# Kernel optimization log

Measured on AMD Instinct MI355X. Metric: run time of the kernel, lower is better.

## Reference

```python
import jax, jax.numpy as jnp
import numpy as np

N_NODES = 100000
N_EDGES = 3200000
N_GRAPHS = 256
NFEAT = 256
NHID = 256
NCLASS = 16


def setup_inputs() -> dict:
    key = jax.random.key(0)
    ks = jax.random.split(key, 8)
    feats = jax.random.normal(ks[0], (N_NODES, NFEAT), dtype=jnp.float32)
    edge_src = jax.random.randint(ks[1], (N_EDGES,), 0, N_NODES, dtype=jnp.int32)
    edge_dst = jax.random.randint(ks[2], (N_EDGES,), 0, N_NODES, dtype=jnp.int32)
    graph_ids = jnp.sort(jax.random.randint(ks[3], (N_NODES,), 0, N_GRAPHS, dtype=jnp.int32))
    def glorot(k, shape):
        lim = float(np.sqrt(6.0 / (shape[0] + shape[1])))
        return jax.random.uniform(k, shape, dtype=jnp.float32, minval=-lim, maxval=lim)
    return {
        "features": feats,
        "edge_src": edge_src,
        "edge_dst": edge_dst,
        "graph_ids": graph_ids,
        "W1": glorot(ks[4], (NFEAT, NHID)), "b1": jnp.zeros((NHID,), jnp.float32),
        "W2": glorot(ks[5], (NHID, NHID)), "b2": jnp.zeros((NHID,), jnp.float32),
        "W3": glorot(ks[6], (NHID, NHID)), "b3": jnp.zeros((NHID,), jnp.float32),
        "Wlin": glorot(ks[7], (NHID, NCLASS)), "blin": jnp.zeros((NCLASS,), jnp.float32),
    }


def _degree_norms(edge_src, edge_dst):
    ones = jnp.ones((N_EDGES,), jnp.float32)
    out_deg = jax.ops.segment_sum(ones, edge_src, num_segments=N_NODES)
    in_deg = jax.ops.segment_sum(ones, edge_dst, num_segments=N_NODES)
    # DGL norm='both': D_out^{-1/2} on source side, D_in^{-1/2} on dest side
    norm_src = jnp.where(out_deg > 0, jax.lax.rsqrt(jnp.maximum(out_deg, 1.0)), 0.0)
    norm_dst = jnp.where(in_deg > 0, jax.lax.rsqrt(jnp.maximum(in_deg, 1.0)), 0.0)
    return norm_src, norm_dst


def _graph_conv(x, W, b, edge_src, edge_dst, norm_src, norm_dst):
    h = x @ W                                  # [N, out]
    msg = (h * norm_src[:, None])[edge_src]    # [E, out] gather
    agg = jax.ops.segment_sum(msg, edge_dst, num_segments=N_NODES)  # scatter-add
    return jax.nn.relu(agg * norm_dst[:, None] + b)


def reference(features, edge_src, edge_dst, graph_ids, W1, b1, W2, b2, W3, b3, Wlin, blin):
    norm_src, norm_dst = _degree_norms(edge_src, edge_dst)
    h = _graph_conv(features, W1, b1, edge_src, edge_dst, norm_src, norm_dst)
    # dropout is identity in eval mode
    h = _graph_conv(h, W2, b2, edge_src, edge_dst, norm_src, norm_dst)
    h = _graph_conv(h, W3, b3, edge_src, edge_dst, norm_src, norm_dst)
    # AvgPooling: mean of node features per graph
    sums = jax.ops.segment_sum(h, graph_ids, num_segments=N_GRAPHS)
    counts = jax.ops.segment_sum(jnp.ones((N_NODES,), jnp.float32), graph_ids, num_segments=N_GRAPHS)
    hg = sums / jnp.maximum(counts, 1.0)[:, None]   # [G, nhid]
    logits = hg @ Wlin + blin                        # [G, nclass]
    return jax.nn.log_softmax(logits, axis=1)
```

## Files before the change

kernel.cpp:

```cpp
#include <hip/hip_runtime.h>
#include <math.h>


#define HID 256

static __device__ __forceinline__ unsigned short f2bf(float f) {
    unsigned int u = __float_as_uint(f);
    unsigned int r = (u + 0x7fff + ((u >> 16) & 1)) >> 16;
    return (unsigned short)r;
}
static __device__ __forceinline__ float bf2f(unsigned short v) {
    return __uint_as_float(((unsigned int)v) << 16);
}

__global__ void k_degree_rank(const int* __restrict__ src, const int* __restrict__ dst,
                              int* __restrict__ outd, int* __restrict__ ind,
                              int* __restrict__ rank, int E) {
    int tid = blockIdx.x * blockDim.x + threadIdx.x;
    int stride = gridDim.x * blockDim.x;
    int E4 = E >> 2;
    const int4* src4 = (const int4*)src;
    const int4* dst4 = (const int4*)dst;
    int4* rank4 = (int4*)rank;
    for (int i = tid; i < E4; i += stride) {
        int4 s = src4[i], d = dst4[i];
        atomicAdd(&outd[s.x], 1); atomicAdd(&outd[s.y], 1);
        atomicAdd(&outd[s.z], 1); atomicAdd(&outd[s.w], 1);
        int4 r;
        r.x = atomicAdd(&ind[d.x], 1);
        r.y = atomicAdd(&ind[d.y], 1);
        r.z = atomicAdd(&ind[d.z], 1);
        r.w = atomicAdd(&ind[d.w], 1);
        rank4[i] = r;
    }
    for (int i = E4 * 4 + tid; i < E; i += stride) {
        atomicAdd(&outd[src[i]], 1);
        rank[i] = atomicAdd(&ind[dst[i]], 1);
    }
}

__global__ __launch_bounds__(256) void k_scan_part(const int* __restrict__ ind,
                                                   int* __restrict__ part, int N) {
    int b = blockIdx.x, t = threadIdx.x;
    int CH = (N + 255) / 256;
    int lo = b * CH, hi = min(N, lo + CH);
    int s = 0;
    for (int i = lo + t; i < hi; i += 256) s += ind[i];
    __shared__ int sm[256];
    sm[t] = s; __syncthreads();
    for (int o = 128; o; o >>= 1) { if (t < o) sm[t] += sm[t + o]; __syncthreads(); }
    if (!t) part[b] = sm[0];
}

__global__ __launch_bounds__(256) void k_scan_top(int* __restrict__ part) {
    int t = threadIdx.x;
    __shared__ int sm[256];
    int v = part[t];
    sm[t] = v; __syncthreads();
    for (int o = 1; o < 256; o <<= 1) {
        int u = (t >= o) ? sm[t - o] : 0;
        __syncthreads();
        sm[t] += u;
        __syncthreads();
    }
    part[t] = sm[t] - v;
}

__global__ __launch_bounds__(256) void k_scan_fill(const int* __restrict__ ind,
                                                   const int* __restrict__ outd,
                                                   const int* __restrict__ part,
                                                   int* __restrict__ offs,
                                                   float* __restrict__ ns,
                                                   float* __restrict__ nd, int N) {
    int b = blockIdx.x, t = threadIdx.x;
    int CH = (N + 255) / 256;
    int lo = b * CH, hi = min(N, lo + CH);
    __shared__ int sm[256];
    int base = part[b];
    for (int s0 = lo; s0 < hi; s0 += 256) {
        int i = s0 + t;
        int v = (i < hi) ? ind[i] : 0;
        sm[t] = v; __syncthreads();
        for (int o = 1; o < 256; o <<= 1) {
            int u = (t >= o) ? sm[t - o] : 0;
            __syncthreads();
            sm[t] += u;
            __syncthreads();
        }
        if (i < hi) {
            offs[i] = base + sm[t] - v;
            int od = outd[i];
            ns[i] = od > 0 ? rsqrtf((float)od) : 0.f;
            nd[i] = v > 0 ? rsqrtf((float)v) : 0.f;
        }
        base += sm[255];
        __syncthreads();
    }
    if (b == 255 && t == 0) offs[N] = base;
}

__global__ void k_fill(const int* __restrict__ src, const int* __restrict__ dst,
                       const int* __restrict__ rank, const int* __restrict__ offs,
                       int* __restrict__ csr, int E) {
    int tid = blockIdx.x * blockDim.x + threadIdx.x;
    int stride = gridDim.x * blockDim.x;
    int E4 = E >> 2;
    const int4* src4 = (const int4*)src;
    const int4* dst4 = (const int4*)dst;
    const int4* rank4 = (const int4*)rank;
    for (int i = tid; i < E4; i += stride) {
        int4 s = src4[i], d = dst4[i], r = rank4[i];
        csr[offs[d.x] + r.x] = s.x;
        csr[offs[d.y] + r.y] = s.y;
        csr[offs[d.z] + r.z] = s.z;
        csr[offs[d.w] + r.w] = s.w;
    }
    for (int i = E4 * 4 + tid; i < E; i += stride)
        csr[offs[dst[i]] + rank[i]] = src[i];
}

__global__ __launch_bounds__(256) void k_gemm(const float* __restrict__ A,
                                              const float* __restrict__ B,
                                              const float* __restrict__ ns,
                                              unsigned short* __restrict__ C, int M) {
    __shared__ float As[16][132];
    __shared__ float Bs[16][132];
    int t = threadIdx.x;
    int tx = t & 15, ty = t >> 4;
    int row0 = blockIdx.x * 128;
    int col0 = blockIdx.y * 128;
    float c[8][8] = {};
    for (int k0 = 0; k0 < 256; k0 += 16) {
        {
            int ar = t >> 1;
            int ak = (t & 1) * 8;
            int grow = row0 + ar;
            float4 a0 = make_float4(0.f, 0.f, 0.f, 0.f), a1 = a0;
            if (grow < M) {
                a0 = *(const float4*)&A[(size_t)grow * 256 + k0 + ak];
                a1 = *(const float4*)&A[(size_t)grow * 256 + k0 + ak + 4];
            }
            As[ak + 0][ar] = a0.x; As[ak + 1][ar] = a0.y;
            As[ak + 2][ar] = a0.z; As[ak + 3][ar] = a0.w;
            As[ak + 4][ar] = a1.x; As[ak + 5][ar] = a1.y;
            As[ak + 6][ar] = a1.z; As[ak + 7][ar] = a1.w;
        }
        {
            int br = t >> 4;
            int bc = (t & 15) * 8;
            float4 b0 = *(const float4*)&B[(size_t)(k0 + br) * 256 + col0 + bc];
            float4 b1 = *(const float4*)&B[(size_t)(k0 + br) * 256 + col0 + bc + 4];
            *(float4*)&Bs[br][bc] = b0;
            *(float4*)&Bs[br][bc + 4] = b1;
        }
        __syncthreads();
#pragma unroll
        for (int k = 0; k < 16; ++k) {
            float a[8], b[8];
            *(float4*)&a[0] = *(float4*)&As[k][ty * 4];
            *(float4*)&a[4] = *(float4*)&As[k][64 + ty * 4];
            *(float4*)&b[0] = *(float4*)&Bs[k][tx * 4];
            *(float4*)&b[4] = *(float4*)&Bs[k][64 + tx * 4];
#pragma unroll
            for (int i = 0; i < 8; ++i)
#pragma unroll
                for (int j = 0; j < 8; ++j)
                    c[i][j] = fmaf(a[i], b[j], c[i][j]);
        }
        __syncthreads();
    }
#pragma unroll
    for (int i = 0; i < 8; ++i) {
        int grow = row0 + ((i < 4) ? (ty * 4 + i) : (64 + ty * 4 + i - 4));
        if (grow < M) {
            float s = ns[grow];
            ushort4 v0, v1;
            v0.x = f2bf(c[i][0] * s); v0.y = f2bf(c[i][1] * s);
            v0.z = f2bf(c[i][2] * s); v0.w = f2bf(c[i][3] * s);
            v1.x = f2bf(c[i][4] * s); v1.y = f2bf(c[i][5] * s);
            v1.z = f2bf(c[i][6] * s); v1.w = f2bf(c[i][7] * s);
            *(ushort4*)&C[(size_t)grow * 256 + col0 + tx * 4] = v0;
            *(ushort4*)&C[(size_t)grow * 256 + col0 + 64 + tx * 4] = v1;
        }
    }
}

__global__ __launch_bounds__(256) void k_agg(const unsigned short* __restrict__ h,
                                             const int* __restrict__ csr,
                                             const int* __restrict__ offs,
                                             const float* __restrict__ nd,
                                             const float* __restrict__ bias,
                                             float* __restrict__ out, int N) {
    int wave = threadIdx.x >> 6;
    int lane = threadIdx.x & 63;
    int node = blockIdx.x * 4 + wave;
    if (node >= N) return;
    int e0 = offs[node], e1 = offs[node + 1];
    float acc0 = 0.f, acc1 = 0.f, acc2 = 0.f, acc3 = 0.f;
    int e = e0;
    for (; e + 1 < e1; e += 2) {
        int s0 = csr[e], s1 = csr[e + 1];
        ushort4 a = *(const ushort4*)&h[(size_t)s0 * 256 + lane * 4];
        ushort4 b = *(const ushort4*)&h[(size_t)s1 * 256 + lane * 4];
        acc0 += bf2f(a.x); acc1 += bf2f(a.y); acc2 += bf2f(a.z); acc3 += bf2f(a.w);
        acc0 += bf2f(b.x); acc1 += bf2f(b.y); acc2 += bf2f(b.z); acc3 += bf2f(b.w);
    }
    if (e < e1) {
        int s0 = csr[e];
        ushort4 a = *(const ushort4*)&h[(size_t)s0 * 256 + lane * 4];
        acc0 += bf2f(a.x); acc1 += bf2f(a.y); acc2 += bf2f(a.z); acc3 += bf2f(a.w);
    }
    float sc = nd[node];
    float4 b4 = *(const float4*)&bias[lane * 4];
    float4 r;
    r.x = fmaxf(fmaf(acc0, sc, b4.x), 0.f);
    r.y = fmaxf(fmaf(acc1, sc, b4.y), 0.f);
    r.z = fmaxf(fmaf(acc2, sc, b4.z), 0.f);
    r.w = fmaxf(fmaf(acc3, sc, b4.w), 0.f);
    *(float4*)&out[(size_t)node * 256 + lane * 4] = r;
}

__global__ __launch_bounds__(256) void k_pool(const float* __restrict__ h,
                                              const int* __restrict__ gid,
                                              const float* __restrict__ Wlin,
                                              const float* __restrict__ blin,
                                              float* __restrict__ out, int N) {
    int g = blockIdx.x;
    int t = threadIdx.x;
    int s, e;
    {
        int lo = 0, hi = N;
        while (lo < hi) { int m = (lo + hi) >> 1; if (gid[m] < g) lo = m + 1; else hi = m; }
        s = lo;
        lo = s; hi = N;
        while (lo < hi) { int m = (lo + hi) >> 1; if (gid[m] < g + 1) lo = m + 1; else hi = m; }
        e = lo;
    }
    float acc = 0.f;
    for (int i = s; i < e; ++i) acc += h[(size_t)i * 256 + t];
    float cntf = (float)((e - s) > 0 ? (e - s) : 1);
    __shared__ float hg[256];
    hg[t] = acc / cntf;
    __syncthreads();
    if (t < 16) {
        float v = blin[t];
        for (int k = 0; k < 256; ++k) v = fmaf(hg[k], Wlin[k * 16 + t], v);
        float m = v;
#pragma unroll
        for (int off = 8; off; off >>= 1) m = fmaxf(m, __shfl_xor(m, off, 16));
        float ex = expf(v - m);
        float ssum = ex;
#pragma unroll
        for (int off = 8; off; off >>= 1) ssum += __shfl_xor(ssum, off, 16);
        out[g * 16 + t] = v - m - logf(ssum);
    }
}

extern "C" void kernel_launch(void* const* d_in, const int* in_sizes, int n_in,
                              void* d_out, int out_size, void* d_ws, size_t ws_size,
                              hipStream_t stream) {
    const float* feats   = (const float*)d_in[0];
    const int*   edge_src= (const int*)d_in[1];
    const int*   edge_dst= (const int*)d_in[2];
    const int*   gid     = (const int*)d_in[3];
    const float* W1 = (const float*)d_in[4];  const float* b1 = (const float*)d_in[5];
    const float* W2 = (const float*)d_in[6];  const float* b2 = (const float*)d_in[7];
    const float* W3 = (const float*)d_in[8];  const float* b3 = (const float*)d_in[9];
    const float* Wlin = (const float*)d_in[10]; const float* blin = (const float*)d_in[11];
    float* out = (float*)d_out;

    const int E = in_sizes[1];
    const int N = in_sizes[3];
    const int G = 256;

    size_t off = 0;
    auto alloc = [&](size_t bytes) -> void* {
        void* p = (char*)d_ws + off;
        off += (bytes + 255) & ~(size_t)255;
        return p;
    };
    int*   outd = (int*)alloc((size_t)N * 4);
    int*   ind  = (int*)alloc((size_t)N * 4);
    size_t zero_bytes = off;
    int*   part = (int*)alloc(256 * 4);
    int*   offs = (int*)alloc(((size_t)N + 1) * 4);
    float* ns   = (float*)alloc((size_t)N * 4);
    float* nd   = (float*)alloc((size_t)N * 4);
    int*   csr  = (int*)alloc((size_t)E * 4);
    unsigned short* htmp = (unsigned short*)alloc((size_t)N * HID * 2);
    float* buf  = (float*)alloc((size_t)N * HID * 4);
    int*   rank = (int*)buf;
    (void)ws_size;

    hipMemsetAsync(d_ws, 0, zero_bytes, stream);

    k_degree_rank<<<2048, 256, 0, stream>>>(edge_src, edge_dst, outd, ind, rank, E);
    k_scan_part<<<256, 256, 0, stream>>>(ind, part, N);
    k_scan_top<<<1, 256, 0, stream>>>(part);
    k_scan_fill<<<256, 256, 0, stream>>>(ind, outd, part, offs, ns, nd, N);
    k_fill<<<2048, 256, 0, stream>>>(edge_src, edge_dst, rank, offs, csr, E);

    dim3 ggrid((N + 127) / 128, 2);
    int agg_blocks = (N + 3) / 4;

    k_gemm<<<ggrid, 256, 0, stream>>>(feats, W1, ns, htmp, N);
    k_agg<<<agg_blocks, 256, 0, stream>>>(htmp, csr, offs, nd, b1, buf, N);
    k_gemm<<<ggrid, 256, 0, stream>>>(buf, W2, ns, htmp, N);
    k_agg<<<agg_blocks, 256, 0, stream>>>(htmp, csr, offs, nd, b2, buf, N);
    k_gemm<<<ggrid, 256, 0, stream>>>(buf, W3, ns, htmp, N);
    k_agg<<<agg_blocks, 256, 0, stream>>>(htmp, csr, offs, nd, b3, buf, N);

    k_pool<<<G, 256, 0, stream>>>(buf, gid, Wlin, blin, out, N);
    (void)out_size;
}
```

Before: 1.771 ms.

## Switch node-feature GEMMs to bf16 MFMA and store hidden activations in bf16

Replaces the FP32 SIMT tiled GEMM with a bf16 MFMA (16x16x32) kernel that reads pre-transposed bf16 weights and bf16 activations. It adds a feature cast kernel and a weight transpose/cast kernel, and changes the aggregation and pooling kernels to write and read bf16 hidden states instead of fp32. The aim is to cut GEMM compute time and halve the activation traffic between layers, at the cost of extra prep passes and reduced input precision. The epilogue writes scalar 2-byte stores, which may coalesce poorly.

```diff
diff --git a/kernel.cpp b/kernel.cpp
--- a/kernel.cpp
+++ b/kernel.cpp
@@ -3,6 +3,10 @@
 
 
 #define HID 256
+
+typedef __attribute__((ext_vector_type(4))) short short4v;
+typedef __attribute__((ext_vector_type(8))) short short8v;
+typedef __attribute__((ext_vector_type(4))) float f32x4;
 
 static __device__ __forceinline__ unsigned short f2bf(float f) {
     unsigned int u = __float_as_uint(f);
@@ -119,68 +123,91 @@
         csr[offs[dst[i]] + rank[i]] = src[i];
 }
 
-__global__ __launch_bounds__(256) void k_gemm(const float* __restrict__ A,
-                                              const float* __restrict__ B,
-                                              const float* __restrict__ ns,
-                                              unsigned short* __restrict__ C, int M) {
-    __shared__ float As[16][132];
-    __shared__ float Bs[16][132];
+__global__ void k_cast(const float* __restrict__ in, unsigned short* __restrict__ out, int n4) {
+    int i = blockIdx.x * blockDim.x + threadIdx.x;
+    int stride = gridDim.x * blockDim.x;
+    for (; i < n4; i += stride) {
+        float4 v = ((const float4*)in)[i];
+        ushort4 o;
+        o.x = f2bf(v.x); o.y = f2bf(v.y); o.z = f2bf(v.z); o.w = f2bf(v.w);
+        ((ushort4*)out)[i] = o;
+    }
+}
+
+__global__ __launch_bounds__(256) void k_wprep(const float* __restrict__ W1,
+                                               const float* __restrict__ W2,
+                                               const float* __restrict__ W3,
+                                               unsigned short* __restrict__ Wt) {
+    int n = blockIdx.x, t = threadIdx.x;
+    Wt[0 * 65536 + n * 256 + t] = f2bf(W1[t * 256 + n]);
+    Wt[1 * 65536 + n * 256 + t] = f2bf(W2[t * 256 + n]);
+    Wt[2 * 65536 + n * 256 + t] = f2bf(W3[t * 256 + n]);
+}
+
+__global__ __launch_bounds__(256) void k_gemm_mf(const unsigned short* __restrict__ A,
+                                                 const unsigned short* __restrict__ Bt,
+                                                 const float* __restrict__ ns,
+                                                 unsigned short* __restrict__ C, int M) {
+    __shared__ unsigned short As[128 * 40];
+    __shared__ unsigned short Bs[128 * 40];
     int t = threadIdx.x;
-    int tx = t & 15, ty = t >> 4;
-    int row0 = blockIdx.x * 128;
-    int col0 = blockIdx.y * 128;
-    float c[8][8] = {};
-    for (int k0 = 0; k0 < 256; k0 += 16) {
-        {
-            int ar = t >> 1;
-            int ak = (t & 1) * 8;
-            int grow = row0 + ar;
-            float4 a0 = make_float4(0.f, 0.f, 0.f, 0.f), a1 = a0;
+    int m0 = blockIdx.x * 128, n0 = blockIdx.y * 128;
+    int w = t >> 6, lane = t & 63;
+    int wr = w >> 1, wc = w & 1;
+    int l15 = lane & 15, l4 = lane >> 4;
+    f32x4 acc[4][4] = {};
+    for (int k0 = 0; k0 < 256; k0 += 32) {
+#pragma unroll
+        for (int j = 0; j < 2; ++j) {
+            int chunk = t + 256 * j;
+            int r = chunk >> 2, q = chunk & 3;
+            int grow = m0 + r;
+            ushort4 v0 = {0, 0, 0, 0}, v1 = {0, 0, 0, 0};
             if (grow < M) {
-                a0 = *(const float4*)&A[(size_t)grow * 256 + k0 + ak];
-                a1 = *(const float4*)&A[(size_t)grow * 256 + k0 + ak + 4];
+                v0 = *(const ushort4*)&A[(size_t)grow * 256 + k0 + q * 8];
+                v1 = *(const ushort4*)&A[(size_t)grow * 256 + k0 + q * 8 + 4];
             }
-            As[ak + 0][ar] = a0.x; As[ak + 1][ar] = a0.y;
-            As[ak + 2][ar] = a0.z; As[ak + 3][ar] = a0.w;
-            As[ak + 4][ar] = a1.x; As[ak + 5][ar] = a1.y;
-            As[ak + 6][ar] = a1.z; As[ak + 7][ar] = a1.w;
-        }
-        {
-            int br = t >> 4;
-            int bc = (t & 15) * 8;
-            float4 b0 = *(const float4*)&B[(size_t)(k0 + br) * 256 + col0 + bc];
-            float4 b1 = *(const float4*)&B[(size_t)(k0 + br) * 256 + col0 + bc + 4];
-            *(float4*)&Bs[br][bc] = b0;
-            *(float4*)&Bs[br][bc + 4] = b1;
-        }
-        __syncthreads();
-#pragma unroll
-        for (int k = 0; k < 16; ++k) {
-            float a[8], b[8];
-            *(float4*)&a[0] = *(float4*)&As[k][ty * 4];
-            *(float4*)&a[4] = *(float4*)&As[k][64 + ty * 4];
-            *(float4*)&b[0] = *(float4*)&Bs[k][tx * 4];
-            *(float4*)&b[4] = *(float4*)&Bs[k][64 + tx * 4];
-#pragma unroll
-            for (int i = 0; i < 8; ++i)
-#pragma unroll
-                for (int j = 0; j < 8; ++j)
-                    c[i][j] = fmaf(a[i], b[j], c[i][j]);
-        }
-        __syncthreads();
-    }
-#pragma unroll
-    for (int i = 0; i < 8; ++i) {
-        int grow = row0 + ((i < 4) ? (ty * 4 + i) : (64 + ty * 4 + i - 4));
-        if (grow < M) {
-            float s = ns[grow];
-            ushort4 v0, v1;
-            v0.x = f2bf(c[i][0] * s); v0.y = f2bf(c[i][1] * s);
-            v0.z = f2bf(c[i][2] * s); v0.w = f2bf(c[i][3] * s);
-            v1.x = f2bf(c[i][4] * s); v1.y = f2bf(c[i][5] * s);
-            v1.z = f2bf(c[i][6] * s); v1.w = f2bf(c[i][7] * s);
-            *(ushort4*)&C[(size_t)grow * 256 + col0 + tx * 4] = v0;
-            *(ushort4*)&C[(size_t)grow * 256 + col0 + 64 + tx * 4] = v1;
+            *(ushort4*)&As[r * 40 + q * 8] = v0;
+            *(ushort4*)&As[r * 40 + q * 8 + 4] = v1;
+            ushort4 u0 = *(const ushort4*)&Bt[(size_t)(n0 + r) * 256 + k0 + q * 8];
+            ushort4 u1 = *(const ushort4*)&Bt[(size_t)(n0 + r) * 256 + k0 + q * 8 + 4];
+            *(ushort4*)&Bs[r * 40 + q * 8] = u0;
+            *(ushort4*)&Bs[r * 40 + q * 8 + 4] = u1;
+        }
+        __syncthreads();
+        short8v af[4], bf[4];
+#pragma unroll
+        for (int f = 0; f < 4; ++f) {
+            int ar = wr * 64 + f * 16 + l15;
+            short4v lo = *(const short4v*)&As[ar * 40 + l4 * 4];
+            short4v hi = *(const short4v*)&As[ar * 40 + l4 * 4 + 16];
+            af[f] = __builtin_shufflevector(lo, hi, 0, 1, 2, 3, 4, 5, 6, 7);
+            int bc = wc * 64 + f * 16 + l15;
+            short4v blo = *(const short4v*)&Bs[bc * 40 + l4 * 4];
+            short4v bhi = *(const short4v*)&Bs[bc * 40 + l4 * 4 + 16];
+            bf[f] = __builtin_shufflevector(blo, bhi, 0, 1, 2, 3, 4, 5, 6, 7);
+        }
+#pragma unroll
+        for (int i = 0; i < 4; ++i)
+#pragma unroll
+            for (int j = 0; j < 4; ++j)
+                acc[i][j] = __builtin_amdgcn_mfma_f32_16x16x32_bf16(af[i], bf[j], acc[i][j], 0, 0, 0);
+        __syncthreads();
+    }
+#pragma unroll
+    for (int i = 0; i < 4; ++i) {
+        int rbase = m0 + wr * 64 + i * 16 + l4 * 4;
+#pragma unroll
+        for (int r = 0; r < 4; ++r) {
+            int row = rbase + r;
+            if (row < M) {
+                float s = ns[row];
+#pragma unroll
+                for (int j = 0; j < 4; ++j) {
+                    int col = n0 + wc * 64 + j * 16 + l15;
+                    C[(size_t)row * 256 + col] = f2bf(acc[i][j][r] * s);
+                }
+            }
         }
     }
 }
@@ -190,7 +217,7 @@
                                              const int* __restrict__ offs,
                                              const float* __restrict__ nd,
                                              const float* __restrict__ bias,
-                                             float* __restrict__ out, int N) {
+                                             unsigned short* __restrict__ out, int N) {
     int wave = threadIdx.x >> 6;
     int lane = threadIdx.x & 63;
     int node = blockIdx.x * 4 + wave;
@@ -212,15 +239,15 @@
     }
     float sc = nd[node];
     float4 b4 = *(const float4*)&bias[lane * 4];
-    float4 r;
-    r.x = fmaxf(fmaf(acc0, sc, b4.x), 0.f);
-    r.y = fmaxf(fmaf(acc1, sc, b4.y), 0.f);
-    r.z = fmaxf(fmaf(acc2, sc, b4.z), 0.f);
-    r.w = fmaxf(fmaf(acc3, sc, b4.w), 0.f);
-    *(float4*)&out[(size_t)node * 256 + lane * 4] = r;
-}
-
-__global__ __launch_bounds__(256) void k_pool(const float* __restrict__ h,
+    ushort4 r;
+    r.x = f2bf(fmaxf(fmaf(acc0, sc, b4.x), 0.f));
+    r.y = f2bf(fmaxf(fmaf(acc1, sc, b4.y), 0.f));
+    r.z = f2bf(fmaxf(fmaf(acc2, sc, b4.z), 0.f));
+    r.w = f2bf(fmaxf(fmaf(acc3, sc, b4.w), 0.f));
+    *(ushort4*)&out[(size_t)node * 256 + lane * 4] = r;
+}
+
+__global__ __launch_bounds__(256) void k_pool(const unsigned short* __restrict__ h,
                                               const int* __restrict__ gid,
                                               const float* __restrict__ Wlin,
                                               const float* __restrict__ blin,
@@ -237,7 +264,7 @@
         e = lo;
     }
     float acc = 0.f;
-    for (int i = s; i < e; ++i) acc += h[(size_t)i * 256 + t];
+    for (int i = s; i < e; ++i) acc += bf2f(h[(size_t)i * 256 + t]);
     float cntf = (float)((e - s) > 0 ? (e - s) : 1);
     __shared__ float hg[256];
     hg[t] = acc / cntf;
@@ -287,9 +314,11 @@
     float* ns   = (float*)alloc((size_t)N * 4);
     float* nd   = (float*)alloc((size_t)N * 4);
     int*   csr  = (int*)alloc((size_t)E * 4);
+    unsigned short* Wt   = (unsigned short*)alloc((size_t)3 * 65536 * 2);
+    unsigned short* fb   = (unsigned short*)alloc((size_t)N * HID * 2);
     unsigned short* htmp = (unsigned short*)alloc((size_t)N * HID * 2);
-    float* buf  = (float*)alloc((size_t)N * HID * 4);
-    int*   rank = (int*)buf;
+    unsigned short* hb   = (unsigned short*)alloc((size_t)N * HID * 2);
+    int*   rank = (int*)hb;
     (void)ws_size;
 
     hipMemsetAsync(d_ws, 0, zero_bytes, stream);
@@ -299,17 +328,19 @@
     k_scan_top<<<1, 256, 0, stream>>>(part);
     k_scan_fill<<<256, 256, 0, stream>>>(ind, outd, part, offs, ns, nd, N);
     k_fill<<<2048, 256, 0, stream>>>(edge_src, edge_dst, rank, offs, csr, E);
+    k_cast<<<2048, 256, 0, stream>>>(feats, fb, N * HID / 4);
+    k_wprep<<<256, 256, 0, stream>>>(W1, W2, W3, Wt);
 
     dim3 ggrid((N + 127) / 128, 2);
     int agg_blocks = (N + 3) / 4;
 
-    k_gemm<<<ggrid, 256, 0, stream>>>(feats, W1, ns, htmp, N);
-    k_agg<<<agg_blocks, 256, 0, stream>>>(htmp, csr, offs, nd, b1, buf, N);
-    k_gemm<<<ggrid, 256, 0, stream>>>(buf, W2, ns, htmp, N);
-    k_agg<<<agg_blocks, 256, 0, stream>>>(htmp, csr, offs, nd, b2, buf, N);
-    k_gemm<<<ggrid, 256, 0, stream>>>(buf, W3, ns, htmp, N);
-    k_agg<<<agg_blocks, 256, 0, stream>>>(htmp, csr, offs, nd, b3, buf, N);
-
-    k_pool<<<G, 256, 0, stream>>>(buf, gid, Wlin, blin, out, N);
+    k_gemm_mf<<<ggrid, 256, 0, stream>>>(fb, Wt + 0 * 65536, ns, htmp, N);
+    k_agg<<<agg_blocks, 256, 0, stream>>>(htmp, csr, offs, nd, b1, hb, N);
+    k_gemm_mf<<<ggrid, 256, 0, stream>>>(hb, Wt + 1 * 65536, ns, htmp, N);
+    k_agg<<<agg_blocks, 256, 0, stream>>>(htmp, csr, offs, nd, b2, hb, N);
+    k_gemm_mf<<<ggrid, 256, 0, stream>>>(hb, Wt + 2 * 65536, ns, htmp, N);
+    k_agg<<<agg_blocks, 256, 0, stream>>>(htmp, csr, offs, nd, b3, hb, N);
+
+    k_pool<<<G, 256, 0, stream>>>(hb, gid, Wlin, blin, out, N);
     (void)out_size;
 }
```

Result: faster. 1.468 ms (-17.1%).
